# Optimization experiments

Measured on AMD Instinct MI355X. Metric: run time of the kernel, lower is better.

## Reference

```python
import jax, jax.numpy as jnp
import numpy as np

GRID, BOXN, LABELN = 14, 2, 20
COORD_RATE, NOOBJ_RATE = 5.0, 0.5
CELL = 1.0 / GRID  # cell_size = 1/grid_num
ALL_BOX = 5 * BOXN


def setup_inputs() -> dict:
    key = jax.random.key(0)
    k1, k2, k3 = jax.random.split(key, 3)
    B = 4096
    C = ALL_BOX + LABELN  # 30
    preds = jax.random.uniform(k1, (B, GRID, GRID, C), dtype=jnp.float32)
    truths = jax.random.uniform(k2, (B, GRID, GRID, C), dtype=jnp.float32)
    objm = jax.random.uniform(k3, (B, GRID, GRID)) < 0.08
    truths = truths.at[..., 4].set(jnp.where(objm, truths[..., 4], 0.0))
    return {"preds": preds, "truths": truths}


def _yolo_loss(preds, truths):
    B = preds.shape[0]
    dt = preds.dtype
    obj = truths[..., 4] > 0                                   # [B,S,S]
    pb = preds[..., :ALL_BOX].reshape(*preds.shape[:3], BOXN, 5)  # [B,S,S,Bx,5]
    tb = truths[..., 0:4]                                       # [B,S,S,4]

    # ---- IoU of every predicted box vs the truth box of its cell ----
    pc = CELL * pb[..., 0:2]; ph = pb[..., 2:4] / 2.0
    tc = CELL * tb[..., 0:2]; th = tb[..., 2:4] / 2.0
    p_lt, p_rb = pc - ph, pc + ph                               # [B,S,S,Bx,2]
    t_lt, t_rb = (tc - th)[..., None, :], (tc + th)[..., None, :]  # [B,S,S,1,2]
    lt = jnp.maximum(p_lt, t_lt)
    rb = jnp.minimum(p_rb, t_rb)
    wh = jnp.clip(rb - lt, 0.0, None)
    inter = wh[..., 0] * wh[..., 1]                             # [B,S,S,Bx]
    pa = (p_rb[..., 0] - p_lt[..., 0]) * (p_rb[..., 1] - p_lt[..., 1])
    ta = (t_rb[..., 0] - t_lt[..., 0]) * (t_rb[..., 1] - t_lt[..., 1])
    ious = inter / (pa + ta - inter)                            # [B,S,S,Bx]

    # ---- responsible-box selection (argmax IoU; ties broken by max conf) ----
    max_iou = jnp.max(ious, axis=-1)                            # [B,S,S]
    tied = ious == max_iou[..., None]
    n_tied = tied.sum(-1)
    conf = pb[..., 4]                                           # [B,S,S,Bx]
    ind_conf = jnp.argmax(jnp.where(tied, conf, -jnp.inf), axis=-1)
    ind_iou = jnp.argmax(ious, axis=-1)
    resp = jnp.where(n_tied > 1, ind_conf, ind_iou)             # [B,S,S]
    resp_oh = jax.nn.one_hot(resp, BOXN, dtype=bool)            # [B,S,S,Bx]

    w_obj = obj.astype(dt)
    pred_resp = jnp.take_along_axis(pb, resp[..., None, None], axis=3)[..., 0, :]  # [B,S,S,5]
    tbox5 = truths[..., 0:5]

    center_loss = jnp.sum(w_obj[..., None] * (pred_resp[..., 0:2] - tbox5[..., 0:2]) ** 2)
    size_loss = jnp.sum(w_obj[..., None] * (jnp.sqrt(pred_resp[..., 2:4]) - jnp.sqrt(tbox5[..., 2:4])) ** 2)
    t_conf = jax.lax.stop_gradient(max_iou)  # .item() in torch detaches the IoU target
    conf_resp_loss = jnp.sum(w_obj * (pred_resp[..., 4] - t_conf) ** 2)
    noresp = (obj[..., None] & (~resp_oh)).astype(dt)
    conf_noresp_loss = jnp.sum(noresp * conf ** 2)
    conf_noobj_loss = jnp.sum((~obj)[..., None].astype(dt) * conf ** 2)
    label_loss = jnp.sum(w_obj[..., None] * (preds[..., ALL_BOX:] - truths[..., ALL_BOX:]) ** 2)

    return (COORD_RATE * (center_loss + size_loss) + conf_resp_loss
            + NOOBJ_RATE * conf_noresp_loss + NOOBJ_RATE * conf_noobj_loss
            + label_loss) / B


def reference(preds, truths):
    return _yolo_loss(preds, truths)
```

## Files before the change

### kernel.cpp

```cpp
#include <hip/hip_runtime.h>
#include <math.h>

#define GRIDN   14
#define BOXN    2
#define LABELN  20
#define ALL_BOX 10
#define CCH     30

#define TCELLS  256
#define TF4     1920
#define VTOT    3840
#define PBLOCKS 512

typedef float vfloat4 __attribute__((ext_vector_type(4)));

__global__ void yolo_zero_kernel(float* out, int n) {
    int i = blockIdx.x * blockDim.x + threadIdx.x;
    if (i < n) out[i] = 0.0f;
}

__device__ __forceinline__ float cell_loss(const float* p, const float* t) {
#pragma clang fp contract(off)
    const float CELL = (float)(1.0 / (double)GRIDN);

    const float tx = t[0], ty = t[1], tw = t[2], th_ = t[3], tconf = t[4];
    const bool obj = tconf > 0.0f;

    const float tcx = CELL * tx, tcy = CELL * ty;
    const float thx = tw * 0.5f, thy = th_ * 0.5f;
    const float tltx = tcx - thx, tlty = tcy - thy;
    const float trbx = tcx + thx, trby = tcy + thy;
    const float ta = (trbx - tltx) * (trby - tlty);

    float iou[BOXN], conf[BOXN];
#pragma unroll
    for (int b = 0; b < BOXN; ++b) {
        const float bx = p[b * 5 + 0], by = p[b * 5 + 1];
        const float bw = p[b * 5 + 2], bh = p[b * 5 + 3];
        conf[b] = p[b * 5 + 4];
        const float pcx = CELL * bx, pcy = CELL * by;
        const float phx = bw * 0.5f, phy = bh * 0.5f;
        const float pltx = pcx - phx, plty = pcy - phy;
        const float prbx = pcx + phx, prby = pcy + phy;
        const float ltx = fmaxf(pltx, tltx), lty = fmaxf(plty, tlty);
        const float rbx = fminf(prbx, trbx), rby = fminf(prby, trby);
        const float whx = fmaxf(rbx - ltx, 0.0f);
        const float why = fmaxf(rby - lty, 0.0f);
        const float inter = whx * why;
        const float pa = (prbx - pltx) * (prby - plty);
        iou[b] = inter / (pa + ta - inter);
    }

    const float max_iou = fmaxf(iou[0], iou[1]);
    bool r1;
    if (iou[0] == iou[1]) r1 = !(conf[0] >= conf[1]);
    else                  r1 = !(iou[0] > iou[1]);

    const float rx = r1 ? p[5] : p[0];
    const float ry = r1 ? p[6] : p[1];
    const float rw = r1 ? p[7] : p[2];
    const float rh = r1 ? p[8] : p[3];
    const float rc = r1 ? p[9] : p[4];

    const float dcx = rx - tx;
    const float dcy = ry - ty;
    const float center = dcx * dcx + dcy * dcy;

    const float dsx = sqrtf(rw) - sqrtf(tw);
    const float dsy = sqrtf(rh) - sqrtf(th_);
    const float size = dsx * dsx + dsy * dsy;

    const float dconf = rc - max_iou;
    const float conf_resp = dconf * dconf;

    const float c_other = r1 ? conf[0] : conf[1];
    const float conf_noresp = c_other * c_other;

    const float conf_noobj = conf[0] * conf[0] + conf[1] * conf[1];

    float label = 0.0f;
#pragma unroll
    for (int k = ALL_BOX; k < CCH; ++k) {
        const float d = p[k] - t[k];
        label += d * d;
    }

    const float w  = obj ? 1.0f : 0.0f;
    const float nw = obj ? 0.0f : 1.0f;
    return w * (5.0f * (center + size) + conf_resp + 0.5f * conf_noresp + label)
         + nw * (0.5f * conf_noobj);
}

__global__ __launch_bounds__(256) void yolo_loss_kernel(
    const float* __restrict__ preds,
    const float* __restrict__ truths,
    float* __restrict__ out,
    int ntiles)
{
#pragma clang fp contract(off)
    __shared__ vfloat4 sbuf[VTOT];
    __shared__ float wsum[4];

    const int tid  = threadIdx.x;
    const int wave = tid >> 6;
    const int lane = tid & 63;

    const vfloat4* pp = (const vfloat4*)preds;
    const vfloat4* tp = (const vfloat4*)truths;

    vfloat4 R[15];
    int tile = blockIdx.x;

    if (tile < ntiles) {
        const long long g = (long long)tile * TF4;
#pragma unroll
        for (int i = 0; i < 15; ++i) {
            const int idx = i * 256 + tid;
            R[i] = (idx < TF4) ? pp[g + idx] : tp[g + (idx - TF4)];
        }
    }

    float acc = 0.0f;
    for (; tile < ntiles; tile += PBLOCKS) {
        const int next = tile + PBLOCKS;

        __syncthreads();
#pragma unroll
        for (int i = 0; i < 15; ++i)
            sbuf[i * 256 + tid] = R[i];

        if (next < ntiles) {
            const long long g = (long long)next * TF4;
#pragma unroll
            for (int i = 0; i < 15; ++i) {
                const int idx = i * 256 + tid;
                R[i] = (idx < TF4) ? pp[g + idx] : tp[g + (idx - TF4)];
            }
        }
        __syncthreads();

        const float* sf = (const float*)sbuf;
        acc += cell_loss(sf + tid * CCH, sf + TF4 * 4 + tid * CCH);
    }

#pragma unroll
    for (int off = 32; off > 0; off >>= 1) acc += __shfl_down(acc, off, 64);
    if (lane == 0) wsum[wave] = acc;
    __syncthreads();
    if (tid == 0) {
        const float s = (wsum[0] + wsum[1]) + (wsum[2] + wsum[3]);
        atomicAdd(out, s * (1.0f / 4096.0f));
    }
}

extern "C" void kernel_launch(void* const* d_in, const int* in_sizes, int n_in,
                              void* d_out, int out_size, void* d_ws, size_t ws_size,
                              hipStream_t stream) {
    const float* preds  = (const float*)d_in[0];
    const float* truths = (const float*)d_in[1];
    float* out = (float*)d_out;

    const int ncells = in_sizes[0] / CCH;
    const int ntiles = ncells / TCELLS;

    yolo_zero_kernel<<<(out_size + 255) / 256, 256, 0, stream>>>(out, out_size);
    yolo_loss_kernel<<<PBLOCKS, 256, 0, stream>>>(preds, truths, out, ntiles);
}
```

Before: 204.4 us.

## Double-buffer LDS tiles with half-size tiles and a single barrier per iteration

Tiles shrink from 256 to 128 cells, and the shared-memory staging buffer becomes two ping-pong halves. Each iteration now needs one __syncthreads instead of two, and only half the threads compute a cell per tile. The aim is to cut barrier stalls and register pressure (8 vfloat4 staging registers instead of 15), with launch bounds hinting two blocks per CU. In exchange there are twice as many loop iterations, fewer bytes in flight per thread, and half the threads sit idle during compute.

```diff
diff --git a/kernel.cpp b/kernel.cpp
--- a/kernel.cpp
+++ b/kernel.cpp
@@ -7,9 +7,10 @@
 #define ALL_BOX 10
 #define CCH     30
 
-#define TCELLS  256
-#define TF4     1920
-#define VTOT    3840
+#define TCELLS  128
+#define TF4     960
+#define VTOT    1920
+#define NREG    8
 #define PBLOCKS 512
 
 typedef float vfloat4 __attribute__((ext_vector_type(4)));
@@ -91,14 +92,14 @@
          + nw * (0.5f * conf_noobj);
 }
 
-__global__ __launch_bounds__(256) void yolo_loss_kernel(
+__global__ __launch_bounds__(256, 2) void yolo_loss_kernel(
     const float* __restrict__ preds,
     const float* __restrict__ truths,
     float* __restrict__ out,
     int ntiles)
 {
 #pragma clang fp contract(off)
-    __shared__ vfloat4 sbuf[VTOT];
+    __shared__ vfloat4 sbuf[2 * VTOT];
     __shared__ float wsum[4];
 
     const int tid  = threadIdx.x;
@@ -108,39 +109,48 @@
     const vfloat4* pp = (const vfloat4*)preds;
     const vfloat4* tp = (const vfloat4*)truths;
 
-    vfloat4 R[15];
+    vfloat4 R[NREG];
     int tile = blockIdx.x;
 
     if (tile < ntiles) {
-        const long long g = (long long)tile * TF4;
+        const int g = tile * TF4;
 #pragma unroll
-        for (int i = 0; i < 15; ++i) {
+        for (int i = 0; i < NREG; ++i) {
             const int idx = i * 256 + tid;
-            R[i] = (idx < TF4) ? pp[g + idx] : tp[g + (idx - TF4)];
+            if (idx < VTOT)
+                R[i] = (idx < TF4) ? pp[g + idx] : tp[g + (idx - TF4)];
         }
     }
 
     float acc = 0.0f;
+    int p = 0;
     for (; tile < ntiles; tile += PBLOCKS) {
-        const int next = tile + PBLOCKS;
+        vfloat4* buf = sbuf + p * VTOT;
+
+#pragma unroll
+        for (int i = 0; i < NREG; ++i) {
+            const int idx = i * 256 + tid;
+            if (idx < VTOT) buf[idx] = R[i];
+        }
 
         __syncthreads();
+
+        const int next = tile + PBLOCKS;
+        if (next < ntiles) {
+            const int g = next * TF4;
 #pragma unroll
-        for (int i = 0; i < 15; ++i)
-            sbuf[i * 256 + tid] = R[i];
-
-        if (next < ntiles) {
-            const long long g = (long long)next * TF4;
-#pragma unroll
-            for (int i = 0; i < 15; ++i) {
+            for (int i = 0; i < NREG; ++i) {
                 const int idx = i * 256 + tid;
-                R[i] = (idx < TF4) ? pp[g + idx] : tp[g + (idx - TF4)];
+                if (idx < VTOT)
+                    R[i] = (idx < TF4) ? pp[g + idx] : tp[g + (idx - TF4)];
             }
         }
-        __syncthreads();
 
-        const float* sf = (const float*)sbuf;
-        acc += cell_loss(sf + tid * CCH, sf + TF4 * 4 + tid * CCH);
+        if (tid < TCELLS) {
+            const float* sf = (const float*)buf;
+            acc += cell_loss(sf + tid * CCH, sf + TF4 * 4 + tid * CCH);
+        }
+        p ^= 1;
     }
 
 #pragma unroll
```

Result: no change. 204.2 us (-0.1%).

## Stream float4 loads directly and evaluate full cell loss only for object cells

Applied to the files above, without the earlier changes.

Removes the shared-memory tile staging and its register double-buffering. Each thread now grid-strides over float4 chunks of preds and truths, adding the no-object confidence term for channels 4 and 9 straight from registers. Only cells whose truth confidence is positive re-gather their 30-channel rows from global memory to compute the full loss, with the no-object term subtracted back out. The intent is fully coalesced streaming with no LDS traffic or barriers, and cheap handling of the mostly empty cells. In exchange, object cells cost scattered re-reads (likely served from cache), the object path diverges within waves, and the summation order changes.

```diff
diff --git a/kernel.cpp b/kernel.cpp
--- a/kernel.cpp
+++ b/kernel.cpp
@@ -7,10 +7,9 @@
 #define ALL_BOX 10
 #define CCH     30
 
-#define TCELLS  256
-#define TF4     1920
-#define VTOT    3840
-#define PBLOCKS 512
+#define NBLK  2048
+#define NTHR  256
+#define GSTRIDE (NBLK * NTHR)
 
 typedef float vfloat4 __attribute__((ext_vector_type(4)));
 
@@ -95,52 +94,47 @@
     const float* __restrict__ preds,
     const float* __restrict__ truths,
     float* __restrict__ out,
-    int ntiles)
+    int nf4)
 {
 #pragma clang fp contract(off)
-    __shared__ vfloat4 sbuf[VTOT];
     __shared__ float wsum[4];
 
     const int tid  = threadIdx.x;
     const int wave = tid >> 6;
     const int lane = tid & 63;
+    const int gid  = blockIdx.x * NTHR + tid;
 
     const vfloat4* pp = (const vfloat4*)preds;
     const vfloat4* tp = (const vfloat4*)truths;
 
-    vfloat4 R[15];
-    int tile = blockIdx.x;
+    float acc = 0.0f;
 
-    if (tile < ntiles) {
-        const long long g = (long long)tile * TF4;
+    for (int idx = gid; idx < nf4; idx += GSTRIDE) {
+        const vfloat4 pv = pp[idx];
+        const vfloat4 tv = tp[idx];
+        const int f  = idx * 4;
+        const int c0 = f % 30;
+
 #pragma unroll
-        for (int i = 0; i < 15; ++i) {
-            const int idx = i * 256 + tid;
-            R[i] = (idx < TF4) ? pp[g + idx] : tp[g + (idx - TF4)];
-        }
-    }
-
-    float acc = 0.0f;
-    for (; tile < ntiles; tile += PBLOCKS) {
-        const int next = tile + PBLOCKS;
-
-        __syncthreads();
-#pragma unroll
-        for (int i = 0; i < 15; ++i)
-            sbuf[i * 256 + tid] = R[i];
-
-        if (next < ntiles) {
-            const long long g = (long long)next * TF4;
-#pragma unroll
-            for (int i = 0; i < 15; ++i) {
-                const int idx = i * 256 + tid;
-                R[i] = (idx < TF4) ? pp[g + idx] : tp[g + (idx - TF4)];
+        for (int j = 0; j < 4; ++j) {
+            int c = c0 + j; if (c >= 30) c -= 30;
+            if (c == 4 || c == 9) {
+                const float v = pv[j];
+                acc += 0.5f * v * v;
             }
         }
-        __syncthreads();
 
-        const float* sf = (const float*)sbuf;
-        acc += cell_loss(sf + tid * CCH, sf + TF4 * 4 + tid * CCH);
+#pragma unroll
+        for (int j = 0; j < 4; ++j) {
+            int c = c0 + j; if (c >= 30) c -= 30;
+            if (c == 4 && tv[j] > 0.0f) {
+                const int cell = (f + j) / 30;
+                const float* p = preds  + cell * CCH;
+                const float* t = truths + cell * CCH;
+                const float p4 = p[4], p9 = p[9];
+                acc += cell_loss(p, t) - 0.5f * (p4 * p4 + p9 * p9);
+            }
+        }
     }
 
 #pragma unroll
@@ -160,9 +154,8 @@
     const float* truths = (const float*)d_in[1];
     float* out = (float*)d_out;
 
-    const int ncells = in_sizes[0] / CCH;
-    const int ntiles = ncells / TCELLS;
+    const int nf4 = in_sizes[0] / 4;
 
     yolo_zero_kernel<<<(out_size + 255) / 256, 256, 0, stream>>>(out, out_size);
-    yolo_loss_kernel<<<PBLOCKS, 256, 0, stream>>>(preds, truths, out, ntiles);
+    yolo_loss_kernel<<<NBLK, NTHR, 0, stream>>>(preds, truths, out, nf4);
 }
```

Result: slower. 225.1 us (+10.1%).
